# Performance work log

Measured on AMD Instinct MI355X. Metric: run time of the kernel, lower is better.

## Reference

```python
import jax, jax.numpy as jnp
import numpy as np

R = 2  # radius from sigma_wh == 1: int((1*6 - 1)/2) = 2 -> fixed 5x5 patch
P = 2 * R + 1

# Design matrix for log-domain Gaussian least-squares fit:
# log z = c0 + c1*x + c2*y + c3*x^2 + c4*y^2
_ys, _xs = np.meshgrid(np.arange(-R, R + 1), np.arange(-R, R + 1), indexing='ij')
_xs = _xs.reshape(-1).astype(np.float32)
_ys = _ys.reshape(-1).astype(np.float32)
_M = np.stack([np.ones_like(_xs), _xs, _ys, _xs ** 2, _ys ** 2], axis=1)  # [25,5]
PINV = jnp.asarray(np.linalg.pinv(_M))  # [5,25]


def _neg_loss(pred, gt):
    pos = (gt == 1.0).astype(pred.dtype)
    neg = (gt < 1.0).astype(pred.dtype)
    neg_w = (1.0 - gt) ** 4
    pos_loss = (jnp.log(pred) * (1.0 - pred) ** 2 * pos).sum()
    neg_loss = (jnp.log(1.0 - pred) * pred ** 2 * neg_w * neg).sum()
    num_pos = pos.sum()
    denom = jnp.where(num_pos == 0, 1.0, num_pos)
    return jnp.where(num_pos == 0, -neg_loss, -(pos_loss + neg_loss) / denom)


def setup_inputs() -> dict:
    key = jax.random.key(0)
    k1, k2, k3, k4 = jax.random.split(key, 4)
    B, C, H, W, O = 8, 80, 128, 128, 128
    return {
        'hm_out': jax.random.normal(k1, (B, C, H, W), jnp.float32),
        'hm_gt': jax.random.uniform(k2, (B, C, H, W), jnp.float32),
        'ct_ind': jax.random.randint(k3, (B, C, O, 2), 0, 124).astype(jnp.int32),
        'sigma_wh': jnp.ones((B, C, O, 2), jnp.float32),
        'hm_mask': jnp.ones((B, C, H, W), jnp.float32),
        'sigmawh_mask': jax.random.randint(k4, (B, C, O), 0, 2).astype(jnp.int32),
    }


def reference(hm_out, hm_gt, ct_ind, sigma_wh, hm_mask, sigmawh_mask):
    B, C, H, W = hm_out.shape
    O = ct_ind.shape[2]

    # --- focal loss (second call in original overwrites the first) ---
    hm_s = jax.nn.sigmoid(hm_out)
    pred = jnp.clip(hm_s, 1e-6, 1.0 - 1e-6)
    focal = _neg_loss(pred, hm_gt * hm_mask)

    # --- batched per-object 5x5 patch gather (replaces python triple loop) ---
    x = jnp.clip(ct_ind[..., 0], R, W - 1 - R)  # [B,C,O]
    y = jnp.clip(ct_ind[..., 1], R, H - 1 - R)
    off = jnp.arange(-R, R + 1)
    yy = y[..., None, None] + off[:, None]            # [B,C,O,P,1]
    xx = x[..., None, None] + off[None, :]            # [B,C,O,1,P]
    b_idx = jnp.arange(B)[:, None, None, None, None]
    c_idx = jnp.arange(C)[None, :, None, None, None]
    patch = hm_s[b_idx, c_idx, yy, xx]                # [B,C,O,P,P]
    logz = jnp.log(patch).reshape(B, C, O, P * P)

    # --- batched gaussian fit: least squares in log domain ---
    coef = jnp.einsum('bcop,kp->bcok', logz, PINV)    # [B,C,O,5]
    bx, by, ax, ay = coef[..., 1], coef[..., 2], coef[..., 3], coef[..., 4]
    ax_s = jnp.where(jnp.abs(ax) < 1e-12, -1.0, ax)
    ay_s = jnp.where(jnp.abs(ay) < 1e-12, -1.0, ay)
    sw2 = -0.5 / ax_s   # fitted variance along w
    sh2 = -0.5 / ay_s   # fitted variance along h
    mu_w = -bx / (2.0 * ax_s)
    mu_h = -by / (2.0 * ay_s)

    # original loop: obj in range(mask.sum()) and mask[obj]==1
    cnt = sigmawh_mask.sum(axis=-1)                                  # [B,C]
    in_loop = jnp.arange(O)[None, None, :] < cnt[..., None]
    valid = (sigmawh_mask == 1) & in_loop & (sw2 > 0) & (sh2 > 0)

    sgw = sigma_wh[..., 0]
    sgh = sigma_wh[..., 1]
    osw = jnp.where(valid, sw2, 1.0)
    osh = jnp.where(valid, sh2, 1.0)
    omw = jnp.where(valid, mu_w, 0.0)
    omh = jnp.where(valid, mu_h, 0.0)
    sgw2 = jnp.where(valid, sgw, 1.0) ** 2
    sgh2 = jnp.where(valid, sgh, 1.0) ** 2

    kl = (0.5 * jnp.log(sgw2 * sgh2 / (osw * osh)) - 1.0
          + 0.5 * (osw / sgw2 + osh / sgh2)
          + 0.5 * (omw ** 2 / sgw2 + omh ** 2 / sgh2))
    kl_sum = jnp.where(valid, kl, 0.0).sum()
    return (kl_sum, focal)
```

## Files before the change

### kernel.cpp

```cpp
#include <hip/hip_runtime.h>
#include <math.h>

#define Bn 8
#define Cn 80
#define Hn 128
#define Wn 128
#define On 128

#define KL_BLOCKS 320
#define FOCAL_BLOCKS 2560
#define FOCAL_STRIDE (FOCAL_BLOCKS * 256)
#define TOTAL_BLOCKS (KL_BLOCKS + FOCAL_BLOCKS)

#define WS_LOSS 0
#define WS_NP FOCAL_BLOCKS
#define WS_KL (2 * FOCAL_BLOCKS)
#define WS_CNT_DBL (2 * FOCAL_BLOCKS + KL_BLOCKS)
#define WS_CNT_BYTES ((size_t)WS_CNT_DBL * 8)

typedef float f32x4 __attribute__((ext_vector_type(4)));

__device__ __forceinline__ f32x4 ldnt(const f32x4* p) {
    return __builtin_nontemporal_load(p);
}

__device__ __forceinline__ void st_agent(double* p, double v) {
    __hip_atomic_store(p, v, __ATOMIC_RELAXED, __HIP_MEMORY_SCOPE_AGENT);
}
__device__ __forceinline__ double ld_agent(const double* p) {
    return __hip_atomic_load(p, __ATOMIC_RELAXED, __HIP_MEMORY_SCOPE_AGENT);
}

__global__ __launch_bounds__(256) void fused_kernel(
    const f32x4* __restrict__ hm_out4, const f32x4* __restrict__ hm_gt4,
    const f32x4* __restrict__ hm_mask4, const float* __restrict__ hm_out,
    const int* __restrict__ ct_ind, const float* __restrict__ sigma_wh,
    const int* __restrict__ sigmawh_mask, double* __restrict__ ws,
    float* __restrict__ out) {
    __shared__ double sd[8];
    __shared__ int si[4];
    __shared__ int last_flag;
    const int t = threadIdx.x;

    if (blockIdx.x >= KL_BLOCKS) {
        const int bid = blockIdx.x - KL_BLOCKS;
        const int i0 = bid * 256 + t;

        float loss = 0.0f, np = 0.0f;

        auto compute = [&](const f32x4& a, const f32x4& g4, const f32x4& m4) {
#pragma unroll
            for (int k = 0; k < 4; ++k) {
                float x = a[k];
                float g = g4[k] * m4[k];
                float e = __expf(-x);
                float tt = 1.0f + e;
                float s = __builtin_amdgcn_rcpf(tt);
                float lt = __logf(tt);
                float om = 1.0f - s;
                float pos_c = -lt * om * om;
                float omg = 1.0f - g;
                float w2 = omg * omg;
                float neg_c = (-x - lt) * (s * s) * (w2 * w2);
                bool is_pos = (g == 1.0f);
                loss += is_pos ? pos_c : ((g < 1.0f) ? neg_c : 0.0f);
                np += is_pos ? 1.0f : 0.0f;
            }
        };

        f32x4 a0 = ldnt(hm_out4 + i0);
        f32x4 g0 = ldnt(hm_gt4 + i0);
        f32x4 m0 = ldnt(hm_mask4 + i0);
        f32x4 a1 = ldnt(hm_out4 + i0 + FOCAL_STRIDE);
        f32x4 g1 = ldnt(hm_gt4 + i0 + FOCAL_STRIDE);
        f32x4 m1 = ldnt(hm_mask4 + i0 + FOCAL_STRIDE);

        f32x4 a2 = ldnt(hm_out4 + i0 + 2 * FOCAL_STRIDE);
        f32x4 g2 = ldnt(hm_gt4 + i0 + 2 * FOCAL_STRIDE);
        f32x4 m2 = ldnt(hm_mask4 + i0 + 2 * FOCAL_STRIDE);
        compute(a0, g0, m0);

        f32x4 a3 = ldnt(hm_out4 + i0 + 3 * FOCAL_STRIDE);
        f32x4 g3 = ldnt(hm_gt4 + i0 + 3 * FOCAL_STRIDE);
        f32x4 m3 = ldnt(hm_mask4 + i0 + 3 * FOCAL_STRIDE);
        compute(a1, g1, m1);

        compute(a2, g2, m2);
        compute(a3, g3, m3);

        for (int off = 32; off > 0; off >>= 1) {
            loss += __shfl_down(loss, off, 64);
            np += __shfl_down(np, off, 64);
        }
        int wave = t >> 6, lane = t & 63;
        if (lane == 0) {
            sd[wave * 2 + 0] = (double)loss;
            sd[wave * 2 + 1] = (double)np;
        }
        __syncthreads();
        if (t == 0) {
            st_agent(&ws[WS_LOSS + bid], sd[0] + sd[2] + sd[4] + sd[6]);
            st_agent(&ws[WS_NP + bid], sd[1] + sd[3] + sd[5] + sd[7]);
        }
    } else {
        const int grp = t >> 7;
        const int o = t & 127;
        const int bc = blockIdx.x * 2 + grp;
        const int wave = t >> 6, lane = t & 63;

        const int m = sigmawh_mask[bc * On + o];
        unsigned long long bal = __ballot(m == 1);
        if (lane == 0) si[wave] = __popcll(bal);
        __syncthreads();
        const int cnt = si[grp * 2] + si[grp * 2 + 1];

        float kl = 0.0f;
        if (m == 1 && o < cnt) {
            int gi = (bc * On + o) * 2;
            int xi = min(max(ct_ind[gi + 0], 2), Wn - 3);
            int yi = min(max(ct_ind[gi + 1], 2), Hn - 3);
            const float* base = hm_out + ((size_t)bc * Hn + yi) * Wn + xi;

            float v[25];
#pragma unroll
            for (int py = 0; py < 5; ++py)
#pragma unroll
                for (int px = 0; px < 5; ++px)
                    v[py * 5 + px] = base[(py - 2) * Wn + (px - 2)];

            float Sbx = 0.f, Sby = 0.f, Sax = 0.f, Say = 0.f;
#pragma unroll
            for (int py = 0; py < 5; ++py) {
#pragma unroll
                for (int px = 0; px < 5; ++px) {
                    float lz = -__logf(1.0f + __expf(-v[py * 5 + px]));
                    float fx = (float)(px - 2), fy = (float)(py - 2);
                    Sbx += fx * lz;
                    Sby += fy * lz;
                    Sax += (fx * fx - 2.0f) * lz;
                    Say += (fy * fy - 2.0f) * lz;
                }
            }
            float bx = Sbx * (1.0f / 50.0f);
            float by = Sby * (1.0f / 50.0f);
            float ax = Sax * (1.0f / 70.0f);
            float ay = Say * (1.0f / 70.0f);

            float ax_s = (fabsf(ax) < 1e-12f) ? -1.0f : ax;
            float ay_s = (fabsf(ay) < 1e-12f) ? -1.0f : ay;
            float sw2 = -0.5f / ax_s;
            float sh2 = -0.5f / ay_s;

            if (sw2 > 0.0f && sh2 > 0.0f) {
                float mw = -bx / (2.0f * ax_s);
                float mh = -by / (2.0f * ay_s);
                float sgw = sigma_wh[gi + 0];
                float sgh = sigma_wh[gi + 1];
                float sgw2 = sgw * sgw;
                float sgh2 = sgh * sgh;
                kl = 0.5f * __logf(sgw2 * sgh2 / (sw2 * sh2)) - 1.0f +
                     0.5f * (sw2 / sgw2 + sh2 / sgh2) +
                     0.5f * (mw * mw / sgw2 + mh * mh / sgh2);
            }
        }

        for (int off = 32; off > 0; off >>= 1) kl += __shfl_down(kl, off, 64);
        if (lane == 0) sd[wave] = (double)kl;
        __syncthreads();
        if (t == 0)
            st_agent(&ws[WS_KL + blockIdx.x], sd[0] + sd[1] + sd[2] + sd[3]);
    }

    if (t == 0) {
        unsigned* cnt_p = (unsigned*)(ws + WS_CNT_DBL);
        asm volatile("s_waitcnt vmcnt(0)" ::: "memory");
        unsigned tick = __hip_atomic_fetch_add(cnt_p, 1u, __ATOMIC_RELAXED,
                                               __HIP_MEMORY_SCOPE_AGENT);
        last_flag = (tick == TOTAL_BLOCKS - 1);
    }
    __syncthreads();
    if (!last_flag) return;

    double L = 0, N = 0, K = 0;
    for (int i = t; i < FOCAL_BLOCKS; i += 256) {
        L += ld_agent(&ws[WS_LOSS + i]);
        N += ld_agent(&ws[WS_NP + i]);
    }
    for (int i = t; i < KL_BLOCKS; i += 256) K += ld_agent(&ws[WS_KL + i]);

    for (int off = 32; off > 0; off >>= 1) {
        L += __shfl_down(L, off, 64);
        N += __shfl_down(N, off, 64);
        K += __shfl_down(K, off, 64);
    }
    __shared__ double fm[4 * 3];
    int wave = t >> 6, lane = t & 63;
    if (lane == 0) {
        fm[wave * 3 + 0] = L;
        fm[wave * 3 + 1] = N;
        fm[wave * 3 + 2] = K;
    }
    __syncthreads();
    if (t == 0) {
        double a = 0, c = 0, d = 0;
#pragma unroll
        for (int w = 0; w < 4; ++w) {
            a += fm[w * 3 + 0];
            c += fm[w * 3 + 1];
            d += fm[w * 3 + 2];
        }
        double denom = (c == 0.0) ? 1.0 : c;
        out[0] = (float)d;
        out[1] = (float)(-a / denom);
    }
}

extern "C" void kernel_launch(void* const* d_in, const int* in_sizes, int n_in,
                              void* d_out, int out_size, void* d_ws,
                              size_t ws_size, hipStream_t stream) {
    const float* hm_out       = (const float*)d_in[0];
    const float* hm_gt        = (const float*)d_in[1];
    const int*   ct_ind       = (const int*)d_in[2];
    const float* sigma_wh     = (const float*)d_in[3];
    const float* hm_mask      = (const float*)d_in[4];
    const int*   sigmawh_mask = (const int*)d_in[5];
    double* ws = (double*)d_ws;
    float* out = (float*)d_out;

    hipMemsetAsync((char*)d_ws + WS_CNT_BYTES, 0, 4, stream);

    fused_kernel<<<TOTAL_BLOCKS, 256, 0, stream>>>(
        (const f32x4*)hm_out, (const f32x4*)hm_gt, (const f32x4*)hm_mask,
        hm_out, ct_ind, sigma_wh, sigmawh_mask, ws, out);
}
```

Baseline: 171.2 us.

## Replace single global last-block reduction with two-level grouped completion counters

Blocks now signal completion on one of 64 per-group counters, each padded to its own 64-byte slot, instead of a single global counter. The last block in each group of 45 reduces that group's partials and adds them with double atomics into global accumulators. A second counter then picks the final group, which writes the outputs. This is meant to cut contention on one atomic and to shorten the serial tail, where one block previously read all 2880 partials; the cost is extra atomics and a larger memset.

After: 149.9 us. 1.14x faster.

```diff
diff --git a/kernel.cpp b/kernel.cpp
--- a/kernel.cpp
+++ b/kernel.cpp
@@ -12,11 +12,18 @@
 #define FOCAL_STRIDE (FOCAL_BLOCKS * 256)
 #define TOTAL_BLOCKS (KL_BLOCKS + FOCAL_BLOCKS)
 
+#define GROUPS 64
+#define GROUP_SIZE 45
+
 #define WS_LOSS 0
 #define WS_NP FOCAL_BLOCKS
 #define WS_KL (2 * FOCAL_BLOCKS)
-#define WS_CNT_DBL (2 * FOCAL_BLOCKS + KL_BLOCKS)
-#define WS_CNT_BYTES ((size_t)WS_CNT_DBL * 8)
+#define CTRL_OFF ((size_t)(2 * FOCAL_BLOCKS + KL_BLOCKS) * 8)
+#define FIN_CNT_OFF (CTRL_OFF + 4096)
+#define ACC_K_OFF (CTRL_OFF + 4160)
+#define ACC_L_OFF (CTRL_OFF + 4224)
+#define ACC_N_OFF (CTRL_OFF + 4288)
+#define CTRL_SIZE 4352
 
 typedef float f32x4 __attribute__((ext_vector_type(4)));
 
@@ -29,6 +36,14 @@
 }
 __device__ __forceinline__ double ld_agent(const double* p) {
     return __hip_atomic_load(p, __ATOMIC_RELAXED, __HIP_MEMORY_SCOPE_AGENT);
+}
+__device__ __forceinline__ unsigned add_agent_u32(unsigned* p, unsigned v) {
+    return __hip_atomic_fetch_add(p, v, __ATOMIC_RELAXED,
+                                  __HIP_MEMORY_SCOPE_AGENT);
+}
+__device__ __forceinline__ void add_agent_f64(double* p, double v) {
+    (void)__hip_atomic_fetch_add(p, v, __ATOMIC_RELAXED,
+                                 __HIP_MEMORY_SCOPE_AGENT);
 }
 
 __global__ __launch_bounds__(256) void fused_kernel(
@@ -39,7 +54,7 @@
     float* __restrict__ out) {
     __shared__ double sd[8];
     __shared__ int si[4];
-    __shared__ int last_flag;
+    __shared__ int grp_win;
     const int t = threadIdx.x;
 
     if (blockIdx.x >= KL_BLOCKS) {
@@ -171,47 +186,47 @@
             st_agent(&ws[WS_KL + blockIdx.x], sd[0] + sd[1] + sd[2] + sd[3]);
     }
 
+    char* wsb = (char*)ws;
+    const int g = blockIdx.x / GROUP_SIZE;
     if (t == 0) {
-        unsigned* cnt_p = (unsigned*)(ws + WS_CNT_DBL);
         asm volatile("s_waitcnt vmcnt(0)" ::: "memory");
-        unsigned tick = __hip_atomic_fetch_add(cnt_p, 1u, __ATOMIC_RELAXED,
-                                               __HIP_MEMORY_SCOPE_AGENT);
-        last_flag = (tick == TOTAL_BLOCKS - 1);
+        unsigned* gc = (unsigned*)(wsb + CTRL_OFF + (size_t)g * 64);
+        unsigned tick = add_agent_u32(gc, 1u);
+        grp_win = (tick == GROUP_SIZE - 1);
     }
     __syncthreads();
-    if (!last_flag) return;
+    if (!grp_win) return;
 
     double L = 0, N = 0, K = 0;
-    for (int i = t; i < FOCAL_BLOCKS; i += 256) {
-        L += ld_agent(&ws[WS_LOSS + i]);
-        N += ld_agent(&ws[WS_NP + i]);
-    }
-    for (int i = t; i < KL_BLOCKS; i += 256) K += ld_agent(&ws[WS_KL + i]);
-
+    if (t < GROUP_SIZE) {
+        int b = g * GROUP_SIZE + t;
+        if (b < KL_BLOCKS) {
+            K = ld_agent(&ws[WS_KL + b]);
+        } else {
+            L = ld_agent(&ws[WS_LOSS + (b - KL_BLOCKS)]);
+            N = ld_agent(&ws[WS_NP + (b - KL_BLOCKS)]);
+        }
+    }
+    if (t >= 64) return;
     for (int off = 32; off > 0; off >>= 1) {
         L += __shfl_down(L, off, 64);
         N += __shfl_down(N, off, 64);
         K += __shfl_down(K, off, 64);
     }
-    __shared__ double fm[4 * 3];
-    int wave = t >> 6, lane = t & 63;
-    if (lane == 0) {
-        fm[wave * 3 + 0] = L;
-        fm[wave * 3 + 1] = N;
-        fm[wave * 3 + 2] = K;
-    }
-    __syncthreads();
     if (t == 0) {
-        double a = 0, c = 0, d = 0;
-#pragma unroll
-        for (int w = 0; w < 4; ++w) {
-            a += fm[w * 3 + 0];
-            c += fm[w * 3 + 1];
-            d += fm[w * 3 + 2];
-        }
-        double denom = (c == 0.0) ? 1.0 : c;
-        out[0] = (float)d;
-        out[1] = (float)(-a / denom);
+        add_agent_f64((double*)(wsb + ACC_K_OFF), K);
+        add_agent_f64((double*)(wsb + ACC_L_OFF), L);
+        add_agent_f64((double*)(wsb + ACC_N_OFF), N);
+        asm volatile("s_waitcnt vmcnt(0)" ::: "memory");
+        unsigned ftick = add_agent_u32((unsigned*)(wsb + FIN_CNT_OFF), 1u);
+        if (ftick == GROUPS - 1) {
+            double Ks = ld_agent((double*)(wsb + ACC_K_OFF));
+            double Ls = ld_agent((double*)(wsb + ACC_L_OFF));
+            double Ns = ld_agent((double*)(wsb + ACC_N_OFF));
+            double denom = (Ns == 0.0) ? 1.0 : Ns;
+            out[0] = (float)Ks;
+            out[1] = (float)(-Ls / denom);
+        }
     }
 }
 
@@ -227,7 +242,7 @@
     double* ws = (double*)d_ws;
     float* out = (float*)d_out;
 
-    hipMemsetAsync((char*)d_ws + WS_CNT_BYTES, 0, 4, stream);
+    hipMemsetAsync((char*)d_ws + CTRL_OFF, 0, CTRL_SIZE, stream);
 
     fused_kernel<<<TOTAL_BLOCKS, 256, 0, stream>>>(
         (const f32x4*)hm_out, (const f32x4*)hm_gt, (const f32x4*)hm_mask,
```
